# Performance work log

Measured on AMD Instinct MI355X. Metric: run time of the kernel, lower is better.

The kernel has to match this reference:

```python
import jax, jax.numpy as jnp
import numpy as np

B, H, W, K = 4, 512, 512, 64
LAMBDA_SEP = 300.0
LAMBDA_MEAN = 300.0


def _huber(d):
    # torch.nn.functional.huber_loss elementwise, delta=1.0
    a = jnp.abs(d)
    return jnp.where(a < 1.0, 0.5 * a * a, a - 0.5)


def setup_inputs() -> dict:
    key = jax.random.key(0)
    k1, k2 = jax.random.split(key)
    prediction = jax.random.normal(k1, (B, 3, H, W), jnp.float32) * 2.0
    # integer instance labels in [0, K); force every instance to appear
    labels = jax.random.randint(k2, (B, H, W), 0, K)
    labels = labels.at[:, 0, :K].set(jnp.arange(K))
    # palette: instance k -> RGB (0, 0, k); id 0 is background (0,0,0)
    target = jnp.zeros((B, 3, H, W), jnp.float32).at[:, 2].set(labels.astype(jnp.float32))
    no_bg = jnp.ones((B,), bool)
    dist_weights = jnp.ones((K, K), jnp.float32)  # distances=None -> all weights 1.0
    palette_ids = jnp.arange(K, dtype=jnp.int32)  # r*65536 + g*256 + b per palette color
    return {"prediction": prediction, "target": target, "no_bg": no_bg,
            "dist_weights": dist_weights, "palette_ids": palette_ids}


def reference(prediction, target, no_bg, dist_weights, palette_ids):
    P = jnp.transpose(prediction, (0, 2, 3, 1)).astype(jnp.float32)  # [B,H,W,3]
    T = jnp.transpose(target, (0, 2, 3, 1))                          # [B,H,W,3]
    Kk = palette_ids.shape[0]
    h, w = P.shape[1], P.shape[2]
    # pixel instance id (exact for small int-valued floats)
    pid = T[..., 0] * 65536.0 + T[..., 1] * 256.0 + T[..., 2]        # [B,H,W]
    masks = (pid[..., None] == palette_ids.astype(pid.dtype)).astype(P.dtype)  # [B,H,W,K]
    counts = masks.sum((1, 2))                                       # [B,K]
    means = jnp.einsum('bhwk,bhwc->bkc', masks, P) / counts[..., None]  # [B,K,3]
    is_bg = palette_ids == 0                                          # [K]
    # bg instance is counted only when no_bg[b] is False
    counted = (~is_bg)[None, :] | (~no_bg)[:, None]                   # [B,K]
    cf = counted.astype(P.dtype)
    # --- intra-instance huber loss (toward instance mean; zeros for bg) ---
    means_z = jnp.where(is_bg[None, :, None], 0.0, means)             # bg target/mean = 0
    mean_pix = jnp.einsum('bhwk,bkc->bhwc', masks, means_z)           # per-pixel target
    hp = _huber(P - mean_pix).sum(-1)                                 # [B,H,W]
    intra_k = jnp.einsum('bhwk,bhw->bk', masks, hp) / (counts * 3.0)  # mean over pix*3
    intra = (intra_k * cf).sum(-1)                                    # [B]
    # --- inter-instance separation (non-bg instances only) ---
    P2 = (P * P).sum(-1)                                              # [B,H,W]
    M2 = (means * means).sum(-1)                                      # [B,K]
    d2 = P2[..., None] + M2[:, None, None, :] - 2.0 * jnp.einsum('bhwc,bkc->bhwk', P, means)
    sep = LAMBDA_SEP / (1.0 + d2)                                     # [B,H,W,K]
    w_pix = jnp.einsum('bhwj,kj->bhwk', masks, dist_weights)          # weight(k, inst(pixel))
    other = 1.0 - masks                                               # pixels not in k
    num = jnp.einsum('bhwk,bhwk,bhwk->bk', sep, w_pix, other)
    n_other = h * w - counts
    inter_k = num / n_other * (10.0 / jnp.sqrt(counts))
    inter = (inter_k * (~is_bg).astype(P.dtype)[None, :]).sum(-1)     # [B]
    # --- mean-level repulsion among counted instance means ---
    diff = means_z[:, :, None, :] - means_z[:, None, :, :]            # [B,K,K,3]
    sqd = (diff * diff).sum(-1)
    pen = dist_weights[None] * LAMBDA_MEAN / (sqd + 1.0)
    triu = jnp.triu(jnp.ones((Kk, Kk), P.dtype), k=1)
    pairmask = cf[:, :, None] * cf[:, None, :] * triu[None]
    npairs = pairmask.sum((1, 2))
    mean_sep = jnp.where(npairs > 0, (pen * pairmask).sum((1, 2)) / jnp.maximum(npairs, 1.0), 0.0)
    ct = jnp.maximum(cf.sum(-1), 1.0)
    loss_b = (intra + inter + mean_sep) / ct
    return jnp.mean(loss_b)
```

## Files before the change

kernel.cpp:

```cpp
#include <hip/hip_runtime.h>

#define KINST 64

__device__ __forceinline__ int decode_k0(float t0, float t1, float t2,
                                         const int* pal_s) {
  int pid = (int)(fmaf(t0, 65536.f, fmaf(t1, 256.f, t2)) + 0.5f);
  if (pid >= 0 && pid < KINST && pal_s[pid] == pid) return pid;
  for (int j = 0; j < KINST; ++j)
    if (pal_s[j] == pid) return j;
  return KINST;
}

__global__ __launch_bounds__(256) void k_stats(const float* __restrict__ pred,
                                               const float* __restrict__ targ,
                                               const int* __restrict__ pal,
                                               float* __restrict__ partialS,
                                               unsigned char* __restrict__ k0c,
                                               int HW) {
  int b = blockIdx.y;
  __shared__ float ls[4][4][KINST];
  __shared__ int pal_s[KINST];
  for (int i = threadIdx.x; i < 4 * 4 * KINST; i += blockDim.x)
    (&ls[0][0][0])[i] = 0.f;
  for (int i = threadIdx.x; i < KINST; i += blockDim.x) pal_s[i] = pal[i];
  __syncthreads();
  int w = threadIdx.x >> 6;
  const float* tb = targ + (size_t)b * 3 * HW;
  const float* pb = pred + (size_t)b * 3 * HW;
  unsigned char* kb = k0c ? k0c + (size_t)b * HW : nullptr;
  int nq = HW >> 2;
  const float4* tb4 = (const float4*)tb;
  const float4* pb4 = (const float4*)pb;
  for (int q = blockIdx.x * blockDim.x + threadIdx.x; q < nq;
       q += gridDim.x * blockDim.x) {
    float4 t0 = tb4[q], t1 = tb4[q + nq], t2 = tb4[q + 2 * nq];
    float4 p0 = pb4[q], p1 = pb4[q + nq], p2 = pb4[q + 2 * nq];
    int ka = decode_k0(t0.x, t1.x, t2.x, pal_s);
    int kc = decode_k0(t0.y, t1.y, t2.y, pal_s);
    int kd = decode_k0(t0.z, t1.z, t2.z, pal_s);
    int ke = decode_k0(t0.w, t1.w, t2.w, pal_s);
    if (ka < KINST) {
      atomicAdd(&ls[w][0][ka], p0.x); atomicAdd(&ls[w][1][ka], p1.x);
      atomicAdd(&ls[w][2][ka], p2.x); atomicAdd(&ls[w][3][ka], 1.f);
    }
    if (kc < KINST) {
      atomicAdd(&ls[w][0][kc], p0.y); atomicAdd(&ls[w][1][kc], p1.y);
      atomicAdd(&ls[w][2][kc], p2.y); atomicAdd(&ls[w][3][kc], 1.f);
    }
    if (kd < KINST) {
      atomicAdd(&ls[w][0][kd], p0.z); atomicAdd(&ls[w][1][kd], p1.z);
      atomicAdd(&ls[w][2][kd], p2.z); atomicAdd(&ls[w][3][kd], 1.f);
    }
    if (ke < KINST) {
      atomicAdd(&ls[w][0][ke], p0.w); atomicAdd(&ls[w][1][ke], p1.w);
      atomicAdd(&ls[w][2][ke], p2.w); atomicAdd(&ls[w][3][ke], 1.f);
    }
    if (kb) {
      uchar4 kk = make_uchar4((unsigned char)ka, (unsigned char)kc,
                              (unsigned char)kd, (unsigned char)ke);
      *(uchar4*)(kb + 4 * (size_t)q) = kk;
    }
  }
  for (int i = (nq << 2) + blockIdx.x * blockDim.x + threadIdx.x; i < HW;
       i += gridDim.x * blockDim.x) {
    int k0 = decode_k0(tb[i], tb[i + HW], tb[i + 2 * HW], pal_s);
    if (kb) kb[i] = (unsigned char)k0;
    if (k0 < KINST) {
      atomicAdd(&ls[w][0][k0], pb[i]); atomicAdd(&ls[w][1][k0], pb[i + HW]);
      atomicAdd(&ls[w][2][k0], pb[i + 2 * HW]); atomicAdd(&ls[w][3][k0], 1.f);
    }
  }
  __syncthreads();
  float* out = partialS + ((size_t)b * gridDim.x + blockIdx.x) * 256;
  int i = threadIdx.x;
  int c = i >> 6, k = i & 63;
  out[i] = ls[0][c][k] + ls[1][c][k] + ls[2][c][k] + ls[3][c][k];
}

__global__ __launch_bounds__(256) void k_reduce(const float* __restrict__ partialS,
                                                const float* __restrict__ dw,
                                                int ndw, int nbs,
                                                float* __restrict__ sums,
                                                int* __restrict__ flagp, int B) {
  int b = blockIdx.x;
  int i = threadIdx.x;
  const float* src = partialS + (size_t)b * nbs * 256;
  float a0 = 0.f, a1 = 0.f, a2 = 0.f, a3 = 0.f;
  int bx = 0;
  #pragma unroll 4
  for (; bx + 4 <= nbs; bx += 4) {
    a0 += src[(size_t)(bx + 0) * 256 + i];
    a1 += src[(size_t)(bx + 1) * 256 + i];
    a2 += src[(size_t)(bx + 2) * 256 + i];
    a3 += src[(size_t)(bx + 3) * 256 + i];
  }
  for (; bx < nbs; ++bx) a0 += src[(size_t)bx * 256 + i];
  float acc = (a0 + a1) + (a2 + a3);
  int c = i >> 6, k = i & 63;
  sums[((size_t)b * KINST + k) * 4 + c] = acc;
  __shared__ int nu_sh;
  if (i == 0) nu_sh = 0;
  __syncthreads();
  int per = (ndw + B - 1) / B;
  int lo = b * per, hi = min(lo + per, ndw);
  float d0 = dw[0];
  int nu = 0;
  for (int x = lo + i; x < hi; x += blockDim.x) nu |= (dw[x] != d0);
  if (nu) atomicOr(&nu_sh, 1);
  __syncthreads();
  if (i == 0) flagp[b] = nu_sh;
}

template <bool USE_CACHE>
__global__ __launch_bounds__(256) void k_pix(const float* __restrict__ pred,
                                             const float* __restrict__ targ,
                                             const unsigned char* __restrict__ k0c,
                                             const int* __restrict__ pal,
                                             const unsigned char* __restrict__ nb_raw,
                                             const float* __restrict__ dw,
                                             const float* __restrict__ sums,
                                             const int* __restrict__ flagp,
                                             float* __restrict__ res_part,
                                             int HW, int B) {
  int b = blockIdx.y;
  __shared__ float4 A_s[KINST + 1];
  __shared__ float4 Z_s[KINST + 1];
  __shared__ float W_s[KINST + 1];
  __shared__ float scale_s[KINST];
  __shared__ float cwN[KINST][KINST + 1];
  __shared__ int pal_s[KINST];
  __shared__ int nonuni_s;
  int t = threadIdx.x;
  if (t < KINST) {
    float4 s = ((const float4*)sums)[b * KINST + t];
    float cnt = s.w;
    float inv = cnt > 0.f ? 1.f / cnt : 0.f;
    float m0 = s.x * inv, m1 = s.y * inv, m2 = s.z * inv;
    bool isbg = (pal[t] == 0);
    bool nb = (nb_raw[b] != 0) || (nb_raw[4 * b] != 0);
    float cf = (!isbg || !nb) ? 1.f : 0.f;
    float sc = (!isbg && cnt > 0.f) ? 10.f / (((float)HW - cnt) * sqrtf(cnt)) : 0.f;
    A_s[t] = make_float4(-2.f * m0, -2.f * m1, -2.f * m2,
                         m0 * m0 + m1 * m1 + m2 * m2 + 1.f);
    Z_s[t] = make_float4(isbg ? 0.f : m0, isbg ? 0.f : m1, isbg ? 0.f : m2,
                         cnt > 0.f ? cf / (3.f * cnt) : 0.f);
    scale_s[t] = sc;
    W_s[t] = 300.f * dw[0] * sc;
    if (!USE_CACHE) pal_s[t] = pal[t];
  }
  if (t == KINST) {
    A_s[KINST] = make_float4(0.f, 0.f, 0.f, 1.f);
    Z_s[KINST] = make_float4(0.f, 0.f, 0.f, 0.f);
    W_s[KINST] = 0.f;
  }
  if (t == 0) {
    int f = 0;
    for (int bb = 0; bb < B; ++bb) f |= flagp[bb];
    nonuni_s = f;
  }
  __syncthreads();
  bool nonuni = nonuni_s != 0;
  if (nonuni) {
    for (int i = t; i < KINST * (KINST + 1); i += blockDim.x) {
      int k = i / (KINST + 1), j = i - k * (KINST + 1);
      float v = 0.f;
      if (j < KINST && j != k) v = 300.f * dw[k * KINST + j] * scale_s[k];
      cwN[k][j] = v;
    }
    __syncthreads();
  }
  const float* pb = pred + (size_t)b * 3 * HW;
  const float* tb = targ + (size_t)b * 3 * HW;
  const float4* pb4 = (const float4*)pb;
  const float4* tb4 = (const float4*)tb;
  int nq = HW >> 2;
  const uchar4* kb4 = USE_CACHE ? (const uchar4*)(k0c + (size_t)b * HW) : nullptr;
  float intra_l = 0.f, inter_l = 0.f;
  for (int q = blockIdx.x * blockDim.x + t; q < nq;
       q += gridDim.x * blockDim.x) {
    float4 P0 = pb4[q], P1 = pb4[q + nq], P2 = pb4[q + 2 * nq];
    int ka, kc, kd, ke;
    if (USE_CACHE) {
      uchar4 kk = kb4[q];
      ka = kk.x; kc = kk.y; kd = kk.z; ke = kk.w;
    } else {
      float4 T0 = tb4[q], T1 = tb4[q + nq], T2 = tb4[q + 2 * nq];
      ka = decode_k0(T0.x, T1.x, T2.x, pal_s);
      kc = decode_k0(T0.y, T1.y, T2.y, pal_s);
      kd = decode_k0(T0.z, T1.z, T2.z, pal_s);
      ke = decode_k0(T0.w, T1.w, T2.w, pal_s);
    }
    float ppa = fmaf(P0.x, P0.x, fmaf(P1.x, P1.x, P2.x * P2.x));
    float ppb = fmaf(P0.y, P0.y, fmaf(P1.y, P1.y, P2.y * P2.y));
    float ppc = fmaf(P0.z, P0.z, fmaf(P1.z, P1.z, P2.z * P2.z));
    float ppd = fmaf(P0.w, P0.w, fmaf(P1.w, P1.w, P2.w * P2.w));
    float aa = 0.f, ab = 0.f, ac = 0.f, ad = 0.f;
    if (!nonuni) {
      #pragma unroll 8
      for (int k = 0; k < KINST; ++k) {
        float4 a = A_s[k];
        float wv = W_s[k];
        float ra = __builtin_amdgcn_rcpf(
            ppa + fmaf(P0.x, a.x, fmaf(P1.x, a.y, fmaf(P2.x, a.z, a.w))));
        float rb = __builtin_amdgcn_rcpf(
            ppb + fmaf(P0.y, a.x, fmaf(P1.y, a.y, fmaf(P2.y, a.z, a.w))));
        float rc = __builtin_amdgcn_rcpf(
            ppc + fmaf(P0.z, a.x, fmaf(P1.z, a.y, fmaf(P2.z, a.z, a.w))));
        float rd = __builtin_amdgcn_rcpf(
            ppd + fmaf(P0.w, a.x, fmaf(P1.w, a.y, fmaf(P2.w, a.z, a.w))));
        aa = fmaf(ra, wv, aa); ab = fmaf(rb, wv, ab);
        ac = fmaf(rc, wv, ac); ad = fmaf(rd, wv, ad);
      }
      {
        float4 a = A_s[ka]; float wv = W_s[ka];
        float r = __builtin_amdgcn_rcpf(
            ppa + fmaf(P0.x, a.x, fmaf(P1.x, a.y, fmaf(P2.x, a.z, a.w))));
        aa = (ka < KINST) ? aa - wv * r : 0.f;
      }
      {
        float4 a = A_s[kc]; float wv = W_s[kc];
        float r = __builtin_amdgcn_rcpf(
            ppb + fmaf(P0.y, a.x, fmaf(P1.y, a.y, fmaf(P2.y, a.z, a.w))));
        ab = (kc < KINST) ? ab - wv * r : 0.f;
      }
      {
        float4 a = A_s[kd]; float wv = W_s[kd];
        float r = __builtin_amdgcn_rcpf(
            ppc + fmaf(P0.z, a.x, fmaf(P1.z, a.y, fmaf(P2.z, a.z, a.w))));
        ac = (kd < KINST) ? ac - wv * r : 0.f;
      }
      {
        float4 a = A_s[ke]; float wv = W_s[ke];
        float r = __builtin_amdgcn_rcpf(
            ppd + fmaf(P0.w, a.x, fmaf(P1.w, a.y, fmaf(P2.w, a.z, a.w))));
        ad = (ke < KINST) ? ad - wv * r : 0.f;
      }
    } else {
      #pragma unroll 4
      for (int k = 0; k < KINST; ++k) {
        float4 a = A_s[k];
        float ra = __builtin_amdgcn_rcpf(
            ppa + fmaf(P0.x, a.x, fmaf(P1.x, a.y, fmaf(P2.x, a.z, a.w))));
        float rb = __builtin_amdgcn_rcpf(
            ppb + fmaf(P0.y, a.x, fmaf(P1.y, a.y, fmaf(P2.y, a.z, a.w))));
        float rc = __builtin_amdgcn_rcpf(
            ppc + fmaf(P0.z, a.x, fmaf(P1.z, a.y, fmaf(P2.z, a.z, a.w))));
        float rd = __builtin_amdgcn_rcpf(
            ppd + fmaf(P0.w, a.x, fmaf(P1.w, a.y, fmaf(P2.w, a.z, a.w))));
        aa = fmaf(ra, cwN[k][ka], aa); ab = fmaf(rb, cwN[k][kc], ab);
        ac = fmaf(rc, cwN[k][kd], ac); ad = fmaf(rd, cwN[k][ke], ad);
      }
    }
    inter_l += (aa + ab) + (ac + ad);
    {
      float4 z = Z_s[ka];
      float q0 = fabsf(P0.x - z.x), q1 = fabsf(P1.x - z.y), q2 = fabsf(P2.x - z.z);
      float hp = (q0 < 1.f ? 0.5f * q0 * q0 : q0 - 0.5f) +
                 (q1 < 1.f ? 0.5f * q1 * q1 : q1 - 0.5f) +
                 (q2 < 1.f ? 0.5f * q2 * q2 : q2 - 0.5f);
      intra_l = fmaf(hp, z.w, intra_l);
    }
    {
      float4 z = Z_s[kc];
      float q0 = fabsf(P0.y - z.x), q1 = fabsf(P1.y - z.y), q2 = fabsf(P2.y - z.z);
      float hp = (q0 < 1.f ? 0.5f * q0 * q0 : q0 - 0.5f) +
                 (q1 < 1.f ? 0.5f * q1 * q1 : q1 - 0.5f) +
                 (q2 < 1.f ? 0.5f * q2 * q2 : q2 - 0.5f);
      intra_l = fmaf(hp, z.w, intra_l);
    }
    {
      float4 z = Z_s[kd];
      float q0 = fabsf(P0.z - z.x), q1 = fabsf(P1.z - z.y), q2 = fabsf(P2.z - z.z);
      float hp = (q0 < 1.f ? 0.5f * q0 * q0 : q0 - 0.5f) +
                 (q1 < 1.f ? 0.5f * q1 * q1 : q1 - 0.5f) +
                 (q2 < 1.f ? 0.5f * q2 * q2 : q2 - 0.5f);
      intra_l = fmaf(hp, z.w, intra_l);
    }
    {
      float4 z = Z_s[ke];
      float q0 = fabsf(P0.w - z.x), q1 = fabsf(P1.w - z.y), q2 = fabsf(P2.w - z.z);
      float hp = (q0 < 1.f ? 0.5f * q0 * q0 : q0 - 0.5f) +
                 (q1 < 1.f ? 0.5f * q1 * q1 : q1 - 0.5f) +
                 (q2 < 1.f ? 0.5f * q2 * q2 : q2 - 0.5f);
      intra_l = fmaf(hp, z.w, intra_l);
    }
  }
  for (int i = (nq << 2) + blockIdx.x * blockDim.x + t; i < HW;
       i += gridDim.x * blockDim.x) {
    float p0 = pb[i], p1 = pb[i + HW], p2 = pb[i + 2 * HW];
    int k0 = USE_CACHE ? (int)k0c[(size_t)b * HW + i]
                       : decode_k0(tb[i], tb[i + HW], tb[i + 2 * HW], pal_s);
    float pp = fmaf(p0, p0, fmaf(p1, p1, p2 * p2));
    float acc = 0.f;
    for (int k = 0; k < KINST; ++k) {
      float4 a = A_s[k];
      float r = __builtin_amdgcn_rcpf(
          pp + fmaf(p0, a.x, fmaf(p1, a.y, fmaf(p2, a.z, a.w))));
      float c = nonuni ? cwN[k][k0] : ((k == k0 || k0 >= KINST) ? 0.f : W_s[k]);
      acc = fmaf(r, c, acc);
    }
    inter_l += acc;
    float4 z = Z_s[k0];
    float q0 = fabsf(p0 - z.x), q1 = fabsf(p1 - z.y), q2 = fabsf(p2 - z.z);
    float hp = (q0 < 1.f ? 0.5f * q0 * q0 : q0 - 0.5f) +
               (q1 < 1.f ? 0.5f * q1 * q1 : q1 - 0.5f) +
               (q2 < 1.f ? 0.5f * q2 * q2 : q2 - 0.5f);
    intra_l = fmaf(hp, z.w, intra_l);
  }
  for (int o = 32; o > 0; o >>= 1) {
    intra_l += __shfl_down(intra_l, o, 64);
    inter_l += __shfl_down(inter_l, o, 64);
  }
  __shared__ float rA[4], rB[4];
  int wid = threadIdx.x >> 6;
  if ((threadIdx.x & 63) == 0) { rA[wid] = intra_l; rB[wid] = inter_l; }
  __syncthreads();
  if (threadIdx.x == 0) {
    float a = 0.f, c = 0.f;
    for (int i = 0; i < 4; ++i) { a += rA[i]; c += rB[i]; }
    float* rp = res_part + ((size_t)b * gridDim.x + blockIdx.x) * 2;
    rp[0] = a; rp[1] = c;
  }
}

__global__ __launch_bounds__(256) void k_final(const float* __restrict__ sums,
                                               const int* __restrict__ pal,
                                               const unsigned char* __restrict__ nb_raw,
                                               const float* __restrict__ dw,
                                               const float* __restrict__ res_part,
                                               int ngx,
                                               float* __restrict__ out,
                                               int B, int HW) {
  __shared__ float4 zf[KINST];
  __shared__ float rA[4], rB[4], rC[4], rD[4], rE[4];
  float total = 0.f;
  for (int b = 0; b < B; ++b) {
    __syncthreads();
    if (threadIdx.x < KINST) {
      int k = threadIdx.x;
      float4 s = ((const float4*)sums)[b * KINST + k];
      float cnt = s.w;
      float inv = cnt > 0.f ? 1.f / cnt : 0.f;
      bool isbg = (pal[k] == 0);
      bool nb = (nb_raw[b] != 0) || (nb_raw[4 * b] != 0);
      float cf = (!isbg || !nb) ? 1.f : 0.f;
      zf[k] = make_float4(isbg ? 0.f : s.x * inv, isbg ? 0.f : s.y * inv,
                          isbg ? 0.f : s.z * inv, cf);
    }
    __syncthreads();
    float psum = 0.f, pcnt = 0.f, cfs = 0.f, ra = 0.f, rc = 0.f;
    for (int idx = threadIdx.x; idx < KINST * KINST; idx += blockDim.x) {
      int j = idx >> 6, k = idx & 63;
      if (j < k) {
        float4 a = zf[j], c4 = zf[k];
        float m = a.w * c4.w;
        float d0 = a.x - c4.x, d1 = a.y - c4.y, d2 = a.z - c4.z;
        float sqd = d0 * d0 + d1 * d1 + d2 * d2;
        psum += dw[j * KINST + k] * 300.f / (sqd + 1.f) * m;
        pcnt += m;
      }
    }
    if (threadIdx.x < KINST) cfs = zf[threadIdx.x].w;
    for (int bx = threadIdx.x; bx < ngx; bx += blockDim.x) {
      const float* rp = res_part + ((size_t)b * ngx + bx) * 2;
      ra += rp[0]; rc += rp[1];
    }
    for (int o = 32; o > 0; o >>= 1) {
      psum += __shfl_down(psum, o, 64);
      pcnt += __shfl_down(pcnt, o, 64);
      cfs += __shfl_down(cfs, o, 64);
      ra += __shfl_down(ra, o, 64);
      rc += __shfl_down(rc, o, 64);
    }
    int wid = threadIdx.x >> 6;
    if ((threadIdx.x & 63) == 0) {
      rA[wid] = psum; rB[wid] = pcnt; rC[wid] = cfs; rD[wid] = ra; rE[wid] = rc;
    }
    __syncthreads();
    if (threadIdx.x == 0) {
      float ps = 0.f, pc = 0.f, cs = 0.f, sa = 0.f, sc2 = 0.f;
      for (int i = 0; i < 4; ++i) {
        ps += rA[i]; pc += rB[i]; cs += rC[i]; sa += rD[i]; sc2 += rE[i];
      }
      float mean_sep = pc > 0.f ? ps / fmaxf(pc, 1.f) : 0.f;
      float ct = fmaxf(cs, 1.f);
      total += (sa + sc2 + mean_sep) / ct;
    }
  }
  if (threadIdx.x == 0) out[0] = total / (float)B;
}

extern "C" void kernel_launch(void* const* d_in, const int* in_sizes, int n_in,
                              void* d_out, int out_size, void* d_ws, size_t ws_size,
                              hipStream_t stream) {
  const float* pred = (const float*)d_in[0];
  const float* targ = (const float*)d_in[1];
  const unsigned char* nb = (const unsigned char*)d_in[2];
  const float* dw = (const float*)d_in[3];
  const int* pal = (const int*)d_in[4];
  int B = in_sizes[2];
  int ndw = in_sizes[3];
  int HW = in_sizes[0] / (3 * B);
  const int GX = 256;

  auto floats_needed = [&](int nbs) -> size_t {
    return (size_t)B * nbs * 256 + (size_t)B * 256 + (size_t)B * GX * 2 + B;
  };
  int nbs = 128;
  bool use_cache = true;
  if (ws_size < floats_needed(128) * 4 + (size_t)B * HW) {
    if (ws_size >= floats_needed(32) * 4 + (size_t)B * HW) nbs = 32;
    else { nbs = 32; use_cache = false; }
  }
  float* partialS = (float*)d_ws;
  float* sums = partialS + (size_t)B * nbs * 256;
  float* res_part = sums + (size_t)B * 256;
  int* flagp = (int*)(res_part + (size_t)B * GX * 2);
  unsigned char* k0c = use_cache ? (unsigned char*)(flagp + B) : nullptr;

  k_stats<<<dim3(nbs, B), 256, 0, stream>>>(pred, targ, pal, partialS, k0c, HW);
  k_reduce<<<B, 256, 0, stream>>>(partialS, dw, ndw, nbs, sums, flagp, B);
  if (use_cache)
    k_pix<true><<<dim3(GX, B), 256, 0, stream>>>(pred, targ, k0c, pal, nb, dw,
                                                 sums, flagp, res_part, HW, B);
  else
    k_pix<false><<<dim3(GX, B), 256, 0, stream>>>(pred, targ, k0c, pal, nb, dw,
                                                  sums, flagp, res_part, HW, B);
  k_final<<<1, 256, 0, stream>>>(sums, pal, nb, dw, res_part, GX,
                                 (float*)d_out, B, HW);
}
```

Baseline: 65.12 us.

## Precompute per-instance coefficients in reduce kernel and read them from global in pixel loop

Moves the per-instance coefficient setup (A, Z, W, and the non-uniform weight table) out of every pixel-kernel block into the single-block-per-batch reduce kernel, which writes them to workspace. The pixel kernel's hot 64-iteration loop now reads A/W via uniform global (scalar) loads instead of LDS, and the non-uniform path indexes a global table. The stats grid is also doubled to 256 blocks per batch. This removes redundant per-block setup and LDS traffic, but relies on scalar/cache loads in the inner loop and adds workspace requirements.

Result: slower. 70.75 us (+8.6%).

```diff
diff --git a/kernel.cpp b/kernel.cpp
--- a/kernel.cpp
+++ b/kernel.cpp
@@ -79,11 +79,21 @@
 
 __global__ __launch_bounds__(256) void k_reduce(const float* __restrict__ partialS,
                                                 const float* __restrict__ dw,
+                                                const int* __restrict__ pal,
+                                                const unsigned char* __restrict__ nb_raw,
                                                 int ndw, int nbs,
                                                 float* __restrict__ sums,
-                                                int* __restrict__ flagp, int B) {
+                                                float4* __restrict__ A_g,
+                                                float* __restrict__ W_g,
+                                                float4* __restrict__ Z_g,
+                                                float* __restrict__ cw_g,
+                                                int* __restrict__ flagp,
+                                                int B, int HW) {
   int b = blockIdx.x;
   int i = threadIdx.x;
+  __shared__ float red[256];
+  __shared__ float scale_sh[KINST];
+  __shared__ int nu_sh;
   const float* src = partialS + (size_t)b * nbs * 256;
   float a0 = 0.f, a1 = 0.f, a2 = 0.f, a3 = 0.f;
   int bx = 0;
@@ -96,19 +106,51 @@
   }
   for (; bx < nbs; ++bx) a0 += src[(size_t)bx * 256 + i];
   float acc = (a0 + a1) + (a2 + a3);
+  red[i] = acc;
   int c = i >> 6, k = i & 63;
   sums[((size_t)b * KINST + k) * 4 + c] = acc;
-  __shared__ int nu_sh;
   if (i == 0) nu_sh = 0;
   __syncthreads();
-  int per = (ndw + B - 1) / B;
-  int lo = b * per, hi = min(lo + per, ndw);
-  float d0 = dw[0];
-  int nu = 0;
-  for (int x = lo + i; x < hi; x += blockDim.x) nu |= (dw[x] != d0);
-  if (nu) atomicOr(&nu_sh, 1);
+  {
+    int per = (ndw + B - 1) / B;
+    int lo = b * per, hi = min(lo + per, ndw);
+    float d0 = dw[0];
+    int nu = 0;
+    for (int x = lo + i; x < hi; x += blockDim.x) nu |= (dw[x] != d0);
+    if (nu) atomicOr(&nu_sh, 1);
+  }
+  if (i < KINST) {
+    float s0 = red[i], s1 = red[64 + i], s2 = red[128 + i], cnt = red[192 + i];
+    float inv = cnt > 0.f ? 1.f / cnt : 0.f;
+    float m0 = s0 * inv, m1 = s1 * inv, m2 = s2 * inv;
+    bool isbg = (pal[i] == 0);
+    bool nb = (nb_raw[b] != 0) || (nb_raw[4 * b] != 0);
+    float cf = (!isbg || !nb) ? 1.f : 0.f;
+    float sc = (!isbg && cnt > 0.f) ? 10.f / (((float)HW - cnt) * sqrtf(cnt)) : 0.f;
+    A_g[b * 65 + i] = make_float4(-2.f * m0, -2.f * m1, -2.f * m2,
+                                  m0 * m0 + m1 * m1 + m2 * m2 + 1.f);
+    Z_g[b * 65 + i] = make_float4(isbg ? 0.f : m0, isbg ? 0.f : m1,
+                                  isbg ? 0.f : m2,
+                                  cnt > 0.f ? cf / (3.f * cnt) : 0.f);
+    W_g[b * 65 + i] = 300.f * dw[0] * sc;
+    scale_sh[i] = sc;
+  }
+  if (i == KINST) {
+    A_g[b * 65 + KINST] = make_float4(0.f, 0.f, 0.f, 1.f);
+    Z_g[b * 65 + KINST] = make_float4(0.f, 0.f, 0.f, 0.f);
+    W_g[b * 65 + KINST] = 0.f;
+  }
   __syncthreads();
   if (i == 0) flagp[b] = nu_sh;
+  if (nu_sh) {
+    float* ct = cw_g + (size_t)b * KINST * 65;
+    for (int t2 = i; t2 < KINST * 65; t2 += blockDim.x) {
+      int kk = t2 / 65, j = t2 - kk * 65;
+      float v = 0.f;
+      if (j < KINST && j != kk) v = 300.f * dw[kk * KINST + j] * scale_sh[kk];
+      ct[t2] = v;
+    }
+  }
 }
 
 template <bool USE_CACHE>
@@ -116,43 +158,27 @@
                                              const float* __restrict__ targ,
                                              const unsigned char* __restrict__ k0c,
                                              const int* __restrict__ pal,
-                                             const unsigned char* __restrict__ nb_raw,
-                                             const float* __restrict__ dw,
-                                             const float* __restrict__ sums,
+                                             const float4* __restrict__ A_g,
+                                             const float* __restrict__ W_g,
+                                             const float4* __restrict__ Z_g,
+                                             const float* __restrict__ cw_g,
                                              const int* __restrict__ flagp,
                                              float* __restrict__ res_part,
                                              int HW, int B) {
   int b = blockIdx.y;
-  __shared__ float4 A_s[KINST + 1];
   __shared__ float4 Z_s[KINST + 1];
-  __shared__ float W_s[KINST + 1];
-  __shared__ float scale_s[KINST];
-  __shared__ float cwN[KINST][KINST + 1];
+  __shared__ float4 A_sl[KINST + 1];
+  __shared__ float W_sl[KINST + 1];
   __shared__ int pal_s[KINST];
   __shared__ int nonuni_s;
+  __shared__ float rA[4], rB[4];
   int t = threadIdx.x;
-  if (t < KINST) {
-    float4 s = ((const float4*)sums)[b * KINST + t];
-    float cnt = s.w;
-    float inv = cnt > 0.f ? 1.f / cnt : 0.f;
-    float m0 = s.x * inv, m1 = s.y * inv, m2 = s.z * inv;
-    bool isbg = (pal[t] == 0);
-    bool nb = (nb_raw[b] != 0) || (nb_raw[4 * b] != 0);
-    float cf = (!isbg || !nb) ? 1.f : 0.f;
-    float sc = (!isbg && cnt > 0.f) ? 10.f / (((float)HW - cnt) * sqrtf(cnt)) : 0.f;
-    A_s[t] = make_float4(-2.f * m0, -2.f * m1, -2.f * m2,
-                         m0 * m0 + m1 * m1 + m2 * m2 + 1.f);
-    Z_s[t] = make_float4(isbg ? 0.f : m0, isbg ? 0.f : m1, isbg ? 0.f : m2,
-                         cnt > 0.f ? cf / (3.f * cnt) : 0.f);
-    scale_s[t] = sc;
-    W_s[t] = 300.f * dw[0] * sc;
-    if (!USE_CACHE) pal_s[t] = pal[t];
-  }
-  if (t == KINST) {
-    A_s[KINST] = make_float4(0.f, 0.f, 0.f, 1.f);
-    Z_s[KINST] = make_float4(0.f, 0.f, 0.f, 0.f);
-    W_s[KINST] = 0.f;
-  }
+  if (t < KINST + 1) {
+    Z_s[t] = Z_g[b * 65 + t];
+    A_sl[t] = A_g[b * 65 + t];
+    W_sl[t] = W_g[b * 65 + t];
+  }
+  if (!USE_CACHE && t < KINST) pal_s[t] = pal[t];
   if (t == 0) {
     int f = 0;
     for (int bb = 0; bb < B; ++bb) f |= flagp[bb];
@@ -160,15 +186,9 @@
   }
   __syncthreads();
   bool nonuni = nonuni_s != 0;
-  if (nonuni) {
-    for (int i = t; i < KINST * (KINST + 1); i += blockDim.x) {
-      int k = i / (KINST + 1), j = i - k * (KINST + 1);
-      float v = 0.f;
-      if (j < KINST && j != k) v = 300.f * dw[k * KINST + j] * scale_s[k];
-      cwN[k][j] = v;
-    }
-    __syncthreads();
-  }
+  const float4* pA = A_g + b * 65;
+  const float* pW = W_g + b * 65;
+  const float* cwb = cw_g + (size_t)b * KINST * 65;
   const float* pb = pred + (size_t)b * 3 * HW;
   const float* tb = targ + (size_t)b * 3 * HW;
   const float4* pb4 = (const float4*)pb;
@@ -198,8 +218,8 @@
     if (!nonuni) {
       #pragma unroll 8
       for (int k = 0; k < KINST; ++k) {
-        float4 a = A_s[k];
-        float wv = W_s[k];
+        float4 a = pA[k];
+        float wv = pW[k];
         float ra = __builtin_amdgcn_rcpf(
             ppa + fmaf(P0.x, a.x, fmaf(P1.x, a.y, fmaf(P2.x, a.z, a.w))));
         float rb = __builtin_amdgcn_rcpf(
@@ -212,25 +232,25 @@
         ac = fmaf(rc, wv, ac); ad = fmaf(rd, wv, ad);
       }
       {
-        float4 a = A_s[ka]; float wv = W_s[ka];
+        float4 a = A_sl[ka]; float wv = W_sl[ka];
         float r = __builtin_amdgcn_rcpf(
             ppa + fmaf(P0.x, a.x, fmaf(P1.x, a.y, fmaf(P2.x, a.z, a.w))));
         aa = (ka < KINST) ? aa - wv * r : 0.f;
       }
       {
-        float4 a = A_s[kc]; float wv = W_s[kc];
+        float4 a = A_sl[kc]; float wv = W_sl[kc];
         float r = __builtin_amdgcn_rcpf(
             ppb + fmaf(P0.y, a.x, fmaf(P1.y, a.y, fmaf(P2.y, a.z, a.w))));
         ab = (kc < KINST) ? ab - wv * r : 0.f;
       }
       {
-        float4 a = A_s[kd]; float wv = W_s[kd];
+        float4 a = A_sl[kd]; float wv = W_sl[kd];
         float r = __builtin_amdgcn_rcpf(
             ppc + fmaf(P0.z, a.x, fmaf(P1.z, a.y, fmaf(P2.z, a.z, a.w))));
         ac = (kd < KINST) ? ac - wv * r : 0.f;
       }
       {
-        float4 a = A_s[ke]; float wv = W_s[ke];
+        float4 a = A_sl[ke]; float wv = W_sl[ke];
         float r = __builtin_amdgcn_rcpf(
             ppd + fmaf(P0.w, a.x, fmaf(P1.w, a.y, fmaf(P2.w, a.z, a.w))));
         ad = (ke < KINST) ? ad - wv * r : 0.f;
@@ -238,7 +258,7 @@
     } else {
       #pragma unroll 4
       for (int k = 0; k < KINST; ++k) {
-        float4 a = A_s[k];
+        float4 a = pA[k];
         float ra = __builtin_amdgcn_rcpf(
             ppa + fmaf(P0.x, a.x, fmaf(P1.x, a.y, fmaf(P2.x, a.z, a.w))));
         float rb = __builtin_amdgcn_rcpf(
@@ -247,8 +267,8 @@
             ppc + fmaf(P0.z, a.x, fmaf(P1.z, a.y, fmaf(P2.z, a.z, a.w))));
         float rd = __builtin_amdgcn_rcpf(
             ppd + fmaf(P0.w, a.x, fmaf(P1.w, a.y, fmaf(P2.w, a.z, a.w))));
-        aa = fmaf(ra, cwN[k][ka], aa); ab = fmaf(rb, cwN[k][kc], ab);
-        ac = fmaf(rc, cwN[k][kd], ac); ad = fmaf(rd, cwN[k][ke], ad);
+        aa = fmaf(ra, cwb[k * 65 + ka], aa); ab = fmaf(rb, cwb[k * 65 + kc], ab);
+        ac = fmaf(rc, cwb[k * 65 + kd], ac); ad = fmaf(rd, cwb[k * 65 + ke], ad);
       }
     }
     inter_l += (aa + ab) + (ac + ad);
@@ -293,10 +313,11 @@
     float pp = fmaf(p0, p0, fmaf(p1, p1, p2 * p2));
     float acc = 0.f;
     for (int k = 0; k < KINST; ++k) {
-      float4 a = A_s[k];
+      float4 a = A_sl[k];
       float r = __builtin_amdgcn_rcpf(
           pp + fmaf(p0, a.x, fmaf(p1, a.y, fmaf(p2, a.z, a.w))));
-      float c = nonuni ? cwN[k][k0] : ((k == k0 || k0 >= KINST) ? 0.f : W_s[k]);
+      float c = nonuni ? cwb[k * 65 + k0]
+                       : ((k == k0 || k0 >= KINST) ? 0.f : W_sl[k]);
       acc = fmaf(r, c, acc);
     }
     inter_l += acc;
@@ -311,7 +332,6 @@
     intra_l += __shfl_down(intra_l, o, 64);
     inter_l += __shfl_down(inter_l, o, 64);
   }
-  __shared__ float rA[4], rB[4];
   int wid = threadIdx.x >> 6;
   if ((threadIdx.x & 63) == 0) { rA[wid] = intra_l; rB[wid] = inter_l; }
   __syncthreads();
@@ -404,11 +424,13 @@
   const int GX = 256;
 
   auto floats_needed = [&](int nbs) -> size_t {
-    return (size_t)B * nbs * 256 + (size_t)B * 256 + (size_t)B * GX * 2 + B;
+    return (size_t)B * nbs * 256 + (size_t)B * 256 + (size_t)B * GX * 2 + B +
+           (size_t)B * 65 * 4 + (size_t)B * 65 + (size_t)B * 65 * 4 +
+           (size_t)B * KINST * 65;
   };
-  int nbs = 128;
+  int nbs = 256;
   bool use_cache = true;
-  if (ws_size < floats_needed(128) * 4 + (size_t)B * HW) {
+  if (ws_size < floats_needed(256) * 4 + (size_t)B * HW) {
     if (ws_size >= floats_needed(32) * 4 + (size_t)B * HW) nbs = 32;
     else { nbs = 32; use_cache = false; }
   }
@@ -416,16 +438,22 @@
   float* sums = partialS + (size_t)B * nbs * 256;
   float* res_part = sums + (size_t)B * 256;
   int* flagp = (int*)(res_part + (size_t)B * GX * 2);
-  unsigned char* k0c = use_cache ? (unsigned char*)(flagp + B) : nullptr;
+  float4* A_g = (float4*)(flagp + B);
+  float* W_g = (float*)(A_g + (size_t)B * 65);
+  float4* Z_g = (float4*)(W_g + (size_t)B * 65);
+  float* cw_g = (float*)(Z_g + (size_t)B * 65);
+  unsigned char* k0c = use_cache ? (unsigned char*)(cw_g + (size_t)B * KINST * 65)
+                                 : nullptr;
 
   k_stats<<<dim3(nbs, B), 256, 0, stream>>>(pred, targ, pal, partialS, k0c, HW);
-  k_reduce<<<B, 256, 0, stream>>>(partialS, dw, ndw, nbs, sums, flagp, B);
+  k_reduce<<<B, 256, 0, stream>>>(partialS, dw, pal, nb, ndw, nbs, sums, A_g,
+                                  W_g, Z_g, cw_g, flagp, B, HW);
   if (use_cache)
-    k_pix<true><<<dim3(GX, B), 256, 0, stream>>>(pred, targ, k0c, pal, nb, dw,
-                                                 sums, flagp, res_part, HW, B);
+    k_pix<true><<<dim3(GX, B), 256, 0, stream>>>(pred, targ, k0c, pal, A_g, W_g,
+                                                 Z_g, cw_g, flagp, res_part, HW, B);
   else
-    k_pix<false><<<dim3(GX, B), 256, 0, stream>>>(pred, targ, k0c, pal, nb, dw,
-                                                  sums, flagp, res_part, HW, B);
+    k_pix<false><<<dim3(GX, B), 256, 0, stream>>>(pred, targ, k0c, pal, A_g, W_g,
+                                                  Z_g, cw_g, flagp, res_part, HW, B);
   k_final<<<1, 256, 0, stream>>>(sums, pal, nb, dw, res_part, GX,
                                  (float*)d_out, B, HW);
 }
```
